# Performance work log

Measured on AMD Instinct MI355X. Metric: run time of the kernel, lower is better.

Reference implementation:

```python
import jax, jax.numpy as jnp
import numpy as np

H = 100      # hidden size
L = 4096     # sequence length


def setup_inputs() -> dict:
    key = jax.random.key(0)
    ks = jax.random.split(key, 11)
    s = 1.0 / np.sqrt(H)
    u = lambda k, sh: jax.random.uniform(k, sh, jnp.float32, -s, s)
    return {
        "input_seq": jax.random.normal(ks[0], (L,), jnp.float32),
        "W_ih_l0": u(ks[1], (4 * H, 1)),
        "W_hh_l0": u(ks[2], (4 * H, H)),
        "b_ih_l0": u(ks[3], (4 * H,)),
        "b_hh_l0": u(ks[4], (4 * H,)),
        "W_ih_l1": u(ks[5], (4 * H, H)),
        "W_hh_l1": u(ks[6], (4 * H, H)),
        "b_ih_l1": u(ks[7], (4 * H,)),
        "b_hh_l1": u(ks[8], (4 * H,)),
        "W_lin": u(ks[9], (1, H)),
        "b_lin": u(ks[10], (1,)),
    }


def _lstm_layer(x, Wih, Whh, bih, bhh):
    # x: [L, B, in] -> hs: [L, B, H]. PyTorch gate order: i, f, g, o.
    h_dim = Wih.shape[0] // 4
    b = bih + bhh

    def step(carry, xt):
        h, c = carry
        gates = xt @ Wih.T + h @ Whh.T + b          # [B, 4H]
        i, f, g, o = jnp.split(gates, 4, axis=-1)
        c = jax.nn.sigmoid(f) * c + jax.nn.sigmoid(i) * jnp.tanh(g)
        h = jax.nn.sigmoid(o) * jnp.tanh(c)
        return (h, c), h

    B = x.shape[1]
    h0 = jnp.zeros((B, h_dim), x.dtype)
    c0 = jnp.zeros((B, h_dim), x.dtype)
    _, hs = jax.lax.scan(step, (h0, c0), x)
    return hs


def reference(input_seq, W_ih_l0, W_hh_l0, b_ih_l0, b_hh_l0,
              W_ih_l1, W_hh_l1, b_ih_l1, b_hh_l1, W_lin, b_lin):
    x = input_seq.reshape(-1, 1, 1)                 # [L, B=1, 1]
    h1 = _lstm_layer(x, W_ih_l0, W_hh_l0, b_ih_l0, b_hh_l0)   # [L,1,H]
    h2 = _lstm_layer(h1, W_ih_l1, W_hh_l1, b_ih_l1, b_hh_l1)  # [L,1,H]
    preds = h2.reshape(h2.shape[0], -1) @ W_lin.T + b_lin      # [L,1]
    return preds[-1]                                 # [1]
```

## Files before the change

### kernel.cpp

```cpp
#include <hip/hip_runtime.h>

#define HH 100
#define LL 4096
#define NT 512

#define WS_H1_FLOATS (LL*128)
#define WS_NEEDED ((size_t)WS_H1_FLOATS*4 + (size_t)LL*4)

typedef float v2f __attribute__((ext_vector_type(2)));
__device__ __forceinline__ v2f fma2(v2f a, v2f b, v2f c) { return __builtin_elementwise_fma(a, b, c); }
__device__ __forceinline__ v2f v2c(float2 f) { v2f r; r.x = f.x; r.y = f.y; return r; }

__device__ __forceinline__ float sigmoidf_(float x) { return 1.0f / (1.0f + __expf(-x)); }
__device__ __forceinline__ float tanhf_(float x)    { return 1.0f - 2.0f / (__expf(2.0f * x) + 1.0f); }

#define DECLROW(n) v2f n##_0,n##_1,n##_2,n##_3,n##_4,n##_5,n##_6,n##_7,n##_8,n##_9,n##_10,n##_11, \
                       n##_12,n##_13,n##_14,n##_15,n##_16,n##_17,n##_18,n##_19,n##_20,n##_21,n##_22,n##_23,n##_24;
#define LOADROW(n, P) { const float2* q2_ = reinterpret_cast<const float2*>(P); \
  n##_0=v2c(q2_[0]);   n##_1=v2c(q2_[1]);   n##_2=v2c(q2_[2]);   n##_3=v2c(q2_[3]);   n##_4=v2c(q2_[4]); \
  n##_5=v2c(q2_[5]);   n##_6=v2c(q2_[6]);   n##_7=v2c(q2_[7]);   n##_8=v2c(q2_[8]);   n##_9=v2c(q2_[9]); \
  n##_10=v2c(q2_[10]); n##_11=v2c(q2_[11]); n##_12=v2c(q2_[12]); n##_13=v2c(q2_[13]); n##_14=v2c(q2_[14]); \
  n##_15=v2c(q2_[15]); n##_16=v2c(q2_[16]); n##_17=v2c(q2_[17]); n##_18=v2c(q2_[18]); n##_19=v2c(q2_[19]); \
  n##_20=v2c(q2_[20]); n##_21=v2c(q2_[21]); n##_22=v2c(q2_[22]); n##_23=v2c(q2_[23]); n##_24=v2c(q2_[24]); }

#define STEP2(j,p,q) { float4 hv = hb4[j]; v2f hl, hh; hl.x=hv.x; hl.y=hv.y; hh.x=hv.z; hh.y=hv.w; \
  a0=fma2(wa_##p,hl,a0); a0=fma2(wa_##q,hh,a0); \
  a1=fma2(wb_##p,hl,a1); a1=fma2(wb_##q,hh,a1); }

#define STEP4(j,p,q) { float4 hv = hb4[j]; v2f hl, hh; hl.x=hv.x; hl.y=hv.y; hh.x=hv.z; hh.y=hv.w; \
  a0=fma2(wa_##p,hl,a0); a0=fma2(wa_##q,hh,a0); \
  a1=fma2(wb_##p,hl,a1); a1=fma2(wb_##q,hh,a1); \
  a2=fma2(wc_##p,hl,a2); a2=fma2(wc_##q,hh,a2); \
  a3=fma2(wd_##p,hl,a3); a3=fma2(wd_##q,hh,a3); }

#define P_LDS_FLOATS 5120

__global__ __attribute__((amdgpu_flat_work_group_size(NT, NT)))
           __attribute__((amdgpu_waves_per_eu(2, 2)))
void lstm_pipe2(const float* __restrict__ x_seq,  const float* __restrict__ Wih0,
                const float* __restrict__ Whh0,   const float* __restrict__ bih0,
                const float* __restrict__ bhh0,   const float* __restrict__ Wih1,
                const float* __restrict__ Whh1,   const float* __restrict__ bih1,
                const float* __restrict__ bhh1,   const float* __restrict__ Wlin,
                const float* __restrict__ blin,   float* __restrict__ ws_h1,
                int* __restrict__ ws_flag,        float* __restrict__ out)
{
    extern __shared__ float lds[];
    const int tid = threadIdx.x;

    if (blockIdx.x == 0) {
        float* x_s   = lds;
        float* h1_s  = lds + 4096;
        float* part0 = lds + 4200;

        const int half = tid & 1;
        const int q    = tid >> 1;
        const bool act = (q < 200);
        const int r0   = act ? 2*q : 0;

        {   const float4* src = reinterpret_cast<const float4*>(x_seq);
            float4* dst = reinterpret_cast<float4*>(x_s);
            for (int i = tid; i < LL/4; i += NT) dst[i] = src[i]; }
        if (tid < 104) h1_s[tid] = 0.0f;

        DECLROW(wa) DECLROW(wb)
        LOADROW(wa, Whh0 + (r0+0)*HH + half*50)
        LOADROW(wb, Whh0 + (r0+1)*HH + half*50)
        float bw0 = 0.f, bw1 = 0.f;
        if (act) {
            if (half == 0) { bw0 = bih0[r0] + bhh0[r0]; bw1 = bih0[r0+1] + bhh0[r0+1]; }
            else           { bw0 = Wih0[r0];            bw1 = Wih0[r0+1]; }
        }
        const float4* hb4 = reinterpret_cast<const float4*>(h1_s + half*52);
        float c0 = 0.0f;
        __syncthreads();

        for (int t = 0; t < LL; ++t) {
            const float xt  = x_s[t];
            const float xvs = half ? xt : 1.0f;
            if (act) {
                v2f a0 = {0.f,0.f}, a1 = {0.f,0.f};
                STEP2(0,0,1)   STEP2(1,2,3)   STEP2(2,4,5)   STEP2(3,6,7)
                STEP2(4,8,9)   STEP2(5,10,11) STEP2(6,12,13) STEP2(7,14,15)
                STEP2(8,16,17) STEP2(9,18,19) STEP2(10,20,21) STEP2(11,22,23)
                { float4 hv = hb4[12]; v2f hl; hl.x = hv.x; hl.y = hv.y;
                  a0 = fma2(wa_24, hl, a0); a1 = fma2(wb_24, hl, a1); }
                float* pw = part0 + half*400 + r0;
                pw[0] = fmaf(bw0, xvs, a0.x + a0.y);
                pw[1] = fmaf(bw1, xvs, a1.x + a1.y);
            }
            __syncthreads();
            if (tid < 100) {
                const int j = tid;
                float G0 = part0[j]       + part0[400 + j];
                float G1 = part0[j + 100] + part0[500 + j];
                float G2 = part0[j + 200] + part0[600 + j];
                float G3 = part0[j + 300] + part0[700 + j];
                c0 = sigmoidf_(G1)*c0 + sigmoidf_(G0)*tanhf_(G2);
                float h = sigmoidf_(G3)*tanhf_(c0);
                h1_s[j + 2*(j >= 50)] = h;
                __hip_atomic_store(&ws_h1[t*128 + j], h, __ATOMIC_RELAXED, __HIP_MEMORY_SCOPE_AGENT);
            }
            __syncthreads();
            if (tid == 0)
                __hip_atomic_store(&ws_flag[t], 1, __ATOMIC_RELEASE, __HIP_MEMORY_SCOPE_AGENT);
        }
    } else {
        float* h1c   = lds;
        float* h2_s  = lds + 104;
        float* part1 = lds + 208;
        float* red   = lds + 1808;

        const bool dotter = (tid < 400);
        const int  c    = dotter ? (tid / 200) : 0;
        const int  rem  = dotter ? (tid % 200) : 0;
        const int  half = rem / 100;
        const int  b    = rem % 100;
        const int  rb   = 4*b;
        const float* mat = c ? Whh1 : Wih1;

        DECLROW(wa) DECLROW(wb) DECLROW(wc) DECLROW(wd)
        LOADROW(wa, mat + (rb+0)*HH + half*50)
        LOADROW(wb, mat + (rb+1)*HH + half*50)
        LOADROW(wc, mat + (rb+2)*HH + half*50)
        LOADROW(wd, mat + (rb+3)*HH + half*50)
        float bw0=0.f, bw1=0.f, bw2=0.f, bw3=0.f;
        if (dotter && c == 0 && half == 0) {
            bw0 = bih1[rb]   + bhh1[rb];
            bw1 = bih1[rb+1] + bhh1[rb+1];
            bw2 = bih1[rb+2] + bhh1[rb+2];
            bw3 = bih1[rb+3] + bhh1[rb+3];
        }
        const float4* hb4 = reinterpret_cast<const float4*>((c ? h2_s : h1c) + half*52);
        const int pbase = half*800 + c*400 + rb;

        const bool gl = (tid >= 400) && (tid < 500);
        const int  j  = tid - 400;
        const float wl = gl ? Wlin[j] : 0.0f;
        float c1 = 0.0f;

        if (tid < 104) { h1c[tid] = 0.0f; h2_s[tid] = 0.0f; }
        __syncthreads();
        if (gl) {
            while (__hip_atomic_load(&ws_flag[0], __ATOMIC_ACQUIRE, __HIP_MEMORY_SCOPE_AGENT) == 0) {}
            float h0 = __hip_atomic_load(&ws_h1[j], __ATOMIC_RELAXED, __HIP_MEMORY_SCOPE_AGENT);
            h1c[j + 2*(j >= 50)] = h0;
            while (__hip_atomic_load(&ws_flag[1], __ATOMIC_ACQUIRE, __HIP_MEMORY_SCOPE_AGENT) == 0) {}
        }
        __syncthreads();

        for (int t = 0; t < LL; ++t) {
            float hnf = 0.0f; int f2v = 1;
            if (gl) {
                const int tp1 = (t+1 < LL) ? t+1 : LL-1;
                const int tp2 = (t+2 < LL) ? t+2 : LL-1;
                hnf = __hip_atomic_load(&ws_h1[tp1*128 + j], __ATOMIC_RELAXED, __HIP_MEMORY_SCOPE_AGENT);
                f2v = __hip_atomic_load(&ws_flag[tp2], __ATOMIC_ACQUIRE, __HIP_MEMORY_SCOPE_AGENT);
            }
            if (dotter) {
                v2f a0 = {0.f,0.f}, a1 = {0.f,0.f}, a2 = {0.f,0.f}, a3 = {0.f,0.f};
                STEP4(0,0,1)   STEP4(1,2,3)   STEP4(2,4,5)   STEP4(3,6,7)
                STEP4(4,8,9)   STEP4(5,10,11) STEP4(6,12,13) STEP4(7,14,15)
                STEP4(8,16,17) STEP4(9,18,19) STEP4(10,20,21) STEP4(11,22,23)
                { float4 hv = hb4[12]; v2f hl; hl.x = hv.x; hl.y = hv.y;
                  a0 = fma2(wa_24, hl, a0); a1 = fma2(wb_24, hl, a1);
                  a2 = fma2(wc_24, hl, a2); a3 = fma2(wd_24, hl, a3); }
                reinterpret_cast<float4*>(part1 + pbase)[0] =
                    make_float4(a0.x + a0.y + bw0, a1.x + a1.y + bw1,
                                a2.x + a2.y + bw2, a3.x + a3.y + bw3);
            }
            __syncthreads();
            if (gl) {
                float G0 = (part1[j]       + part1[800+j])       + (part1[400+j]       + part1[1200+j]);
                float G1 = (part1[j+100]   + part1[900+j])       + (part1[500+j]       + part1[1300+j]);
                float G2 = (part1[j+200]   + part1[1000+j])      + (part1[600+j]       + part1[1400+j]);
                float G3 = (part1[j+300]   + part1[1100+j])      + (part1[700+j]       + part1[1500+j]);
                c1 = sigmoidf_(G1)*c1 + sigmoidf_(G0)*tanhf_(G2);
                h2_s[j + 2*(j >= 50)] = sigmoidf_(G3)*tanhf_(c1);
                h1c[j + 2*(j >= 50)] = hnf;
                while (f2v == 0) {
                    const int tp2 = (t+2 < LL) ? t+2 : LL-1;
                    f2v = __hip_atomic_load(&ws_flag[tp2], __ATOMIC_ACQUIRE, __HIP_MEMORY_SCOPE_AGENT);
                }
            }
            __syncthreads();
        }
        if (gl) red[j] = wl * h2_s[j + 2*(j >= 50)];
        __syncthreads();
        if (tid == 0) {
            float s = blin[0];
            for (int k = 0; k < HH; ++k) s += red[k];
            out[0] = s;
        }
    }
}

#define NLDSROW 176
#define RB0  176
#define WQ_OFF   4096
#define H1_OFF   (WQ_OFF + 2*NLDSROW*52)
#define H2_OFF   (H1_OFF + 104)
#define PART_OFF (H2_OFF + 104)
#define Q_OFF    (PART_OFF + 2048)
#define LDS_FLOATS (Q_OFF + 352)

#define TSK(j) { float4 wv = tp4[j]; float4 hv = hb4t[j]; v2f wl_,wh_,hl_,hh_; \
  wl_.x=wv.x; wl_.y=wv.y; wh_.x=wv.z; wh_.y=wv.w; hl_.x=hv.x; hl_.y=hv.y; hh_.x=hv.z; hh_.y=hv.w; \
  tq=fma2(wl_,hl_,tq); tq=fma2(wh_,hh_,tq); }

__global__ __attribute__((amdgpu_flat_work_group_size(NT, NT)))
           __attribute__((amdgpu_waves_per_eu(2, 2)))
void lstm_v256_kernel(const float* __restrict__ x_seq, const float* __restrict__ Wih0,
                      const float* __restrict__ Whh0,  const float* __restrict__ bih0,
                      const float* __restrict__ bhh0,  const float* __restrict__ Wih1,
                      const float* __restrict__ Whh1,  const float* __restrict__ bih1,
                      const float* __restrict__ bhh1,  const float* __restrict__ Wlin,
                      const float* __restrict__ blin,  float* __restrict__ out)
{
    extern __shared__ float lds[];
    float* x_s    = lds;
    float* wq     = lds + WQ_OFF;
    float* h1_s   = lds + H1_OFF;
    float* h2_s   = lds + H2_OFF;
    float* part_s = lds + PART_OFF;
    float* q_s    = lds + Q_OFF;

    const int tid  = threadIdx.x;
    const int half = tid & 1;
    const int qid  = tid >> 1;
    const int rowbase = RB0 + 4*qid;

    {   const float4* src = reinterpret_cast<const float4*>(x_seq);
        float4* dst = reinterpret_cast<float4*>(x_s);
        for (int i = tid; i < LL/4; i += NT) dst[i] = src[i]; }
    for (int idx = tid; idx < 2*NLDSROW*50; idx += NT) {
        int hf  = idx / (NLDSROW*50);
        int rem = idx - hf*(NLDSROW*50);
        int row = rem / 50;
        int cc  = rem - row*50;
        wq[(hf*NLDSROW + row)*52 + cc] = Whh0[row*HH + hf*50 + cc];
    }
    if (tid < 104) { h1_s[tid] = 0.0f; h2_s[tid] = 0.0f; }

    const float* M; int r0;
    if (rowbase < 400)      { M = Whh0; r0 = rowbase; }
    else if (rowbase < 800) { M = Wih1; r0 = rowbase - 400; }
    else                    { M = Whh1; r0 = rowbase - 800; }

    DECLROW(wa) DECLROW(wb) DECLROW(wc) DECLROW(wd)
    LOADROW(wa, M + (r0+0)*HH + half*50)
    LOADROW(wb, M + (r0+1)*HH + half*50)
    LOADROW(wc, M + (r0+2)*HH + half*50)
    LOADROW(wd, M + (r0+3)*HH + half*50)

    float bw0, bw1, bw2, bw3;
    {
        const int ra = rowbase, rb = rowbase+1, rc = rowbase+2, rd = rowbase+3;
        if (half == 0) {
            bw0 = (ra < 400) ? (bih0[ra] + bhh0[ra]) : (ra < 800) ? (bih1[ra-400] + bhh1[ra-400]) : 0.0f;
            bw1 = (rb < 400) ? (bih0[rb] + bhh0[rb]) : (rb < 800) ? (bih1[rb-400] + bhh1[rb-400]) : 0.0f;
            bw2 = (rc < 400) ? (bih0[rc] + bhh0[rc]) : (rc < 800) ? (bih1[rc-400] + bhh1[rc-400]) : 0.0f;
            bw3 = (rd < 400) ? (bih0[rd] + bhh0[rd]) : (rd < 800) ? (bih1[rd-400] + bhh1[rd-400]) : 0.0f;
        } else {
            bw0 = (ra < 400) ? Wih0[ra] : 0.0f;
            bw1 = (rb < 400) ? Wih0[rb] : 0.0f;
            bw2 = (rc < 400) ? Wih0[rc] : 0.0f;
            bw3 = (rd < 400) ? Wih0[rd] : 0.0f;
        }
    }

    float lb = 0.0f;
    if (tid < 2*NLDSROW) lb = half ? Wih0[qid] : (bih0[qid] + bhh0[qid]);
    const float4* tp4  = reinterpret_cast<const float4*>(wq + (half*NLDSROW + qid)*52);
    const float4* hb4t = reinterpret_cast<const float4*>(h1_s + half*52);
    const float4* hb4  = reinterpret_cast<const float4*>(((rowbase < 800) ? h1_s : h2_s) + half*52);

    const float wl = (tid < HH) ? Wlin[tid] : 0.0f;
    const int slotbase = qid + half*1024;
    float c0 = 0.0f, c1 = 0.0f;
    __syncthreads();

    for (int t = 0; t <= LL; ++t) {
        const float xt  = x_s[(t < LL) ? t : (LL-1)];
        const float xvs = half ? xt : 1.0f;
        {
            v2f a0 = {0.f,0.f}, a1 = {0.f,0.f}, a2 = {0.f,0.f}, a3 = {0.f,0.f};
            STEP4(0,0,1)   STEP4(1,2,3)   STEP4(2,4,5)   STEP4(3,6,7)
            STEP4(4,8,9)   STEP4(5,10,11) STEP4(6,12,13) STEP4(7,14,15)
            STEP4(8,16,17) STEP4(9,18,19) STEP4(10,20,21) STEP4(11,22,23)
            { float4 hv = hb4[12]; v2f hl; hl.x = hv.x; hl.y = hv.y;
              a0 = fma2(wa_24, hl, a0); a1 = fma2(wb_24, hl, a1);
              a2 = fma2(wc_24, hl, a2); a3 = fma2(wd_24, hl, a3); }
            part_s[slotbase + 0*256] = fmaf(bw0, xvs, a0.x + a0.y);
            part_s[slotbase + 1*256] = fmaf(bw1, xvs, a1.x + a1.y);
            part_s[slotbase + 2*256] = fmaf(bw2, xvs, a2.x + a2.y);
            part_s[slotbase + 3*256] = fmaf(bw3, xvs, a3.x + a3.y);
        }
        if (tid < 2*NLDSROW) {
            v2f tq = {0.f,0.f};
            TSK(0) TSK(1) TSK(2) TSK(3) TSK(4) TSK(5)
            TSK(6) TSK(7) TSK(8) TSK(9) TSK(10) TSK(11)
            { float4 wv = tp4[12]; float4 hv = hb4t[12];
              v2f wl_, hl_; wl_.x = wv.x; wl_.y = wv.y; hl_.x = hv.x; hl_.y = hv.y;
              tq = fma2(wl_, hl_, tq); }
            q_s[qid + half*NLDSROW] = fmaf(lb, xvs, tq.x + tq.y);
        }
        __syncthreads();
        if (tid < HH) {
            const int jj = tid;
            float g[4];
            #pragma unroll
            for (int k = 0; k < 4; ++k) {
                int r = jj + k*100;
                if (r < NLDSROW) g[k] = q_s[r] + q_s[r + NLDSROW];
                else { int rr = r - RB0; int bb = (rr >> 2) + ((rr & 3) << 8);
                       g[k] = part_s[bb] + part_s[bb + 1024]; }
            }
            if (t < LL) {
                c0 = sigmoidf_(g[1])*c0 + sigmoidf_(g[0])*tanhf_(g[2]);
                h1_s[jj + 2*(jj >= 50)] = sigmoidf_(g[3])*tanhf_(c0);
            }
        } else if (tid >= 128 && tid < 128 + HH) {
            if (t >= 1) {
                const int jj = tid - 128;
                float v[4];
                #pragma unroll
                for (int k = 0; k < 4; ++k) {
                    int g1i = jj + k*100;
                    int rr1 = (400 + g1i) - RB0; int b1i = (rr1 >> 2) + ((rr1 & 3) << 8);
                    int rr2 = (800 + g1i) - RB0; int b2i = (rr2 >> 2) + ((rr2 & 3) << 8);
                    v[k] = (part_s[b1i] + part_s[b1i + 1024]) + (part_s[b2i] + part_s[b2i + 1024]);
                }
                c1 = sigmoidf_(v[1])*c1 + sigmoidf_(v[0])*tanhf_(v[2]);
                h2_s[jj + 2*(jj >= 50)] = sigmoidf_(v[3])*tanhf_(c1);
            }
        }
        __syncthreads();
    }
    if (tid < HH) part_s[tid] = wl * h2_s[tid + 2*(tid >= 50)];
    __syncthreads();
    if (tid == 0) {
        float s = 0.0f;
        for (int k = 0; k < HH; ++k) s += part_s[k];
        out[0] = s + blin[0];
    }
}

extern "C" void kernel_launch(void* const* d_in, const int* in_sizes, int n_in,
                              void* d_out, int out_size, void* d_ws, size_t ws_size,
                              hipStream_t stream) {
    (void)in_sizes; (void)n_in; (void)out_size;

    const float* x_seq = (const float*)d_in[0];
    const float* Wih0  = (const float*)d_in[1];
    const float* Whh0  = (const float*)d_in[2];
    const float* bih0  = (const float*)d_in[3];
    const float* bhh0  = (const float*)d_in[4];
    const float* Wih1  = (const float*)d_in[5];
    const float* Whh1  = (const float*)d_in[6];
    const float* bih1  = (const float*)d_in[7];
    const float* bhh1  = (const float*)d_in[8];
    const float* Wlin  = (const float*)d_in[9];
    const float* blin  = (const float*)d_in[10];
    float* out = (float*)d_out;

    if (d_ws != nullptr && ws_size >= WS_NEEDED) {
        float* ws_h1  = (float*)d_ws;
        int*   ws_flg = (int*)((char*)d_ws + (size_t)WS_H1_FLOATS*4);
        hipMemsetAsync(ws_flg, 0, LL*sizeof(int), stream);
        hipLaunchKernelGGL(lstm_pipe2, dim3(2), dim3(NT),
                           P_LDS_FLOATS*sizeof(float), stream,
                           x_seq, Wih0, Whh0, bih0, bhh0,
                           Wih1, Whh1, bih1, bhh1, Wlin, blin,
                           ws_h1, ws_flg, out);
    } else {
        static bool attr_set = false;
        if (!attr_set) {
            hipFuncSetAttribute((const void*)lstm_v256_kernel,
                                hipFuncAttributeMaxDynamicSharedMemorySize,
                                LDS_FLOATS * (int)sizeof(float));
            attr_set = true;
        }
        hipLaunchKernelGGL(lstm_v256_kernel, dim3(1), dim3(NT),
                           LDS_FLOATS * sizeof(float), stream,
                           x_seq, Wih0, Whh0, bih0, bhh0,
                           Wih1, Whh1, bih1, bhh1, Wlin, blin, out);
    }
}
```

Before: 4.281 ms.

## Split layer-1 LSTM into separate input-projection and recurrent blocks in a 3-stage pipeline

Moves from a two-block pipeline to three blocks. Block 0 runs the layer-0 recurrence. Block 1 computes the layer-1 input projection (Wih1·h1) and streams the pre-activations through a ring buffer in global memory. Block 2 runs only the layer-1 recurrent matvec (Whh1·h2) plus the gate math. The goal is to halve the per-step work on the layer-1 critical path, which previously did both matvecs with four rows per thread. In exchange it adds a second inter-block handoff with acquire/release flags, ring-buffer backpressure counters, and extra global traffic of 800 floats per step. The fallback single-block kernel is also removed.

```diff
diff --git a/kernel.cpp b/kernel.cpp
--- a/kernel.cpp
+++ b/kernel.cpp
@@ -3,9 +3,8 @@
 #define HH 100
 #define LL 4096
 #define NT 512
-
-#define WS_H1_FLOATS (LL*128)
-#define WS_NEEDED ((size_t)WS_H1_FLOATS*4 + (size_t)LL*4)
+#define RH 512
+#define BPLAG 504
 
 typedef float v2f __attribute__((ext_vector_type(2)));
 __device__ __forceinline__ v2f fma2(v2f a, v2f b, v2f c) { return __builtin_elementwise_fma(a, b, c); }
@@ -26,14 +25,229 @@
 #define STEP2(j,p,q) { float4 hv = hb4[j]; v2f hl, hh; hl.x=hv.x; hl.y=hv.y; hh.x=hv.z; hh.y=hv.w; \
   a0=fma2(wa_##p,hl,a0); a0=fma2(wa_##q,hh,a0); \
   a1=fma2(wb_##p,hl,a1); a1=fma2(wb_##q,hh,a1); }
+#define DOT2TAIL { float4 hv = hb4[12]; v2f hl; hl.x = hv.x; hl.y = hv.y; \
+  a0 = fma2(wa_24, hl, a0); a1 = fma2(wb_24, hl, a1); }
+#define DOT2ALL  STEP2(0,0,1) STEP2(1,2,3) STEP2(2,4,5) STEP2(3,6,7) STEP2(4,8,9) STEP2(5,10,11) \
+                 STEP2(6,12,13) STEP2(7,14,15) STEP2(8,16,17) STEP2(9,18,19) STEP2(10,20,21) STEP2(11,22,23) DOT2TAIL
+
+#define AST(p,v) __hip_atomic_store((p), (v), __ATOMIC_RELAXED, __HIP_MEMORY_SCOPE_AGENT)
+#define ALD(p)   __hip_atomic_load((p), __ATOMIC_RELAXED, __HIP_MEMORY_SCOPE_AGENT)
+#define AFLAGST(p) __hip_atomic_store((p), 1, __ATOMIC_RELEASE, __HIP_MEMORY_SCOPE_AGENT)
+#define AFLAGLD(p) __hip_atomic_load((p), __ATOMIC_ACQUIRE, __HIP_MEMORY_SCOPE_AGENT)
+
+#define P3_LDS_FLOATS 5120
+
+__global__ __attribute__((amdgpu_flat_work_group_size(NT, NT)))
+           __attribute__((amdgpu_waves_per_eu(2, 2)))
+void lstm_pipe3(const float* __restrict__ x_seq,  const float* __restrict__ Wih0,
+                const float* __restrict__ Whh0,   const float* __restrict__ bih0,
+                const float* __restrict__ bhh0,   const float* __restrict__ Wih1,
+                const float* __restrict__ Whh1,   const float* __restrict__ bih1,
+                const float* __restrict__ bhh1,   const float* __restrict__ Wlin,
+                const float* __restrict__ blin,
+                float* __restrict__ ws_h1,  float* __restrict__ ws_p01,
+                int* __restrict__ flag0,    int* __restrict__ flag1,
+                int* __restrict__ cons1,    int* __restrict__ cons2,
+                float* __restrict__ out)
+{
+    extern __shared__ float lds[];
+    const int tid  = threadIdx.x;
+    const int half = tid & 1;
+    const int q    = tid >> 1;
+    const bool act = (q < 200);
+    const int r0   = act ? 2*q : 0;
+
+    if (blockIdx.x == 0) {
+        float* x_s   = lds;
+        float* h1_s  = lds + 4096;
+        float* part0 = lds + 4200;
+
+        {   const float4* src = reinterpret_cast<const float4*>(x_seq);
+            float4* dst = reinterpret_cast<float4*>(x_s);
+            for (int i = tid; i < LL/4; i += NT) dst[i] = src[i]; }
+        if (tid < 104) h1_s[tid] = 0.0f;
+
+        DECLROW(wa) DECLROW(wb)
+        LOADROW(wa, Whh0 + (r0+0)*HH + half*50)
+        LOADROW(wb, Whh0 + (r0+1)*HH + half*50)
+        float bw0 = 0.f, bw1 = 0.f;
+        if (act) {
+            if (half == 0) { bw0 = bih0[r0] + bhh0[r0]; bw1 = bih0[r0+1] + bhh0[r0+1]; }
+            else           { bw0 = Wih0[r0];            bw1 = Wih0[r0+1]; }
+        }
+        const float4* hb4 = reinterpret_cast<const float4*>(h1_s + half*52);
+        float c0 = 0.0f;
+        __syncthreads();
+
+        for (int t = 0; t < LL; ++t) {
+            const float xt  = x_s[t];
+            const float xvs = half ? xt : 1.0f;
+            if (act) {
+                v2f a0 = {0.f,0.f}, a1 = {0.f,0.f};
+                DOT2ALL
+                float* pw = part0 + half*400 + r0;
+                pw[0] = fmaf(bw0, xvs, a0.x + a0.y);
+                pw[1] = fmaf(bw1, xvs, a1.x + a1.y);
+            }
+            __syncthreads();
+            if (tid < 100) {
+                const int j = tid;
+                float G0 = part0[j]       + part0[400 + j];
+                float G1 = part0[j + 100] + part0[500 + j];
+                float G2 = part0[j + 200] + part0[600 + j];
+                float G3 = part0[j + 300] + part0[700 + j];
+                c0 = sigmoidf_(G1)*c0 + sigmoidf_(G0)*tanhf_(G2);
+                float h = sigmoidf_(G3)*tanhf_(c0);
+                h1_s[j + 2*(j >= 50)] = h;
+                AST(&ws_h1[(t & (RH-1))*128 + j], h);
+            }
+            __syncthreads();
+            if (tid == 0) {
+                AFLAGST(&flag0[t]);
+                if (t >= BPLAG + 1) {
+                    while (ALD(cons1) < t - BPLAG) {}
+                }
+            }
+        }
+    } else if (blockIdx.x == 1) {
+        float* h1c = lds;
+
+        DECLROW(wa) DECLROW(wb)
+        LOADROW(wa, Wih1 + (r0+0)*HH + half*50)
+        LOADROW(wb, Wih1 + (r0+1)*HH + half*50)
+        float bw0 = 0.f, bw1 = 0.f;
+        if (act && half == 0) { bw0 = bih1[r0] + bhh1[r0]; bw1 = bih1[r0+1] + bhh1[r0+1]; }
+
+        const bool gl = (tid >= 400) && (tid < 500);
+        const int  j  = tid - 400;
+        if (tid < 104) h1c[tid] = 0.0f;
+        __syncthreads();
+
+        if (gl) {
+            while (AFLAGLD(&flag0[0]) == 0) {}
+            h1c[j + 2*(j >= 50)] = ALD(&ws_h1[j]);
+            while (AFLAGLD(&flag0[1]) == 0) {}
+        }
+        __syncthreads();
+        const float4* hb4 = reinterpret_cast<const float4*>(h1c + half*52);
+
+        for (int t = 0; t < LL; ++t) {
+            float hnf = 0.0f; int f2v = 1;
+            if (gl) {
+                const int tp1 = (t+1 < LL) ? t+1 : LL-1;
+                const int tp2 = (t+2 < LL) ? t+2 : LL-1;
+                hnf = ALD(&ws_h1[(tp1 & (RH-1))*128 + j]);
+                f2v = AFLAGLD(&flag0[tp2]);
+            }
+            if (act) {
+                v2f a0 = {0.f,0.f}, a1 = {0.f,0.f};
+                DOT2ALL
+                const int base = (t & (RH-1))*800 + half*400 + r0;
+                AST(&ws_p01[base],     a0.x + a0.y + bw0);
+                AST(&ws_p01[base + 1], a1.x + a1.y + bw1);
+            }
+            __syncthreads();
+            if (gl) {
+                h1c[j + 2*(j >= 50)] = hnf;
+                while (f2v == 0) {
+                    const int tp2 = (t+2 < LL) ? t+2 : LL-1;
+                    f2v = AFLAGLD(&flag0[tp2]);
+                }
+            }
+            if (tid == 0) {
+                AFLAGST(&flag1[t]);
+                AST(cons1, t);
+                if (t >= BPLAG + 1) {
+                    while (ALD(cons2) < t - BPLAG) {}
+                }
+            }
+            __syncthreads();
+        }
+    } else {
+        float* h2_s  = lds;
+        float* part2 = lds + 104;
+        float* red   = lds + 904;
+
+        DECLROW(wa) DECLROW(wb)
+        LOADROW(wa, Whh1 + (r0+0)*HH + half*50)
+        LOADROW(wb, Whh1 + (r0+1)*HH + half*50)
+
+        const bool gl = (tid >= 400) && (tid < 500);
+        const int  j  = tid - 400;
+        const float wl = gl ? Wlin[j] : 0.0f;
+        float c1 = 0.0f;
+        float pc0=0.f,pc1=0.f,pc2=0.f,pc3=0.f,pc4=0.f,pc5=0.f,pc6=0.f,pc7=0.f;
+
+        if (tid < 104) h2_s[tid] = 0.0f;
+        __syncthreads();
+
+        if (gl) {
+            while (AFLAGLD(&flag1[0]) == 0) {}
+            pc0 = ALD(&ws_p01[j]);        pc1 = ALD(&ws_p01[100 + j]);
+            pc2 = ALD(&ws_p01[200 + j]);  pc3 = ALD(&ws_p01[300 + j]);
+            pc4 = ALD(&ws_p01[400 + j]);  pc5 = ALD(&ws_p01[500 + j]);
+            pc6 = ALD(&ws_p01[600 + j]);  pc7 = ALD(&ws_p01[700 + j]);
+            while (AFLAGLD(&flag1[1]) == 0) {}
+        }
+        __syncthreads();
+        const float4* hb4 = reinterpret_cast<const float4*>(h2_s + half*52);
+
+        for (int t = 0; t < LL; ++t) {
+            float pn0=0.f,pn1=0.f,pn2=0.f,pn3=0.f,pn4=0.f,pn5=0.f,pn6=0.f,pn7=0.f;
+            int f2v = 1;
+            if (gl) {
+                const int tp1 = (t+1 < LL) ? t+1 : LL-1;
+                const int tp2 = (t+2 < LL) ? t+2 : LL-1;
+                const int b = (tp1 & (RH-1))*800;
+                pn0 = ALD(&ws_p01[b + j]);        pn1 = ALD(&ws_p01[b + 100 + j]);
+                pn2 = ALD(&ws_p01[b + 200 + j]);  pn3 = ALD(&ws_p01[b + 300 + j]);
+                pn4 = ALD(&ws_p01[b + 400 + j]);  pn5 = ALD(&ws_p01[b + 500 + j]);
+                pn6 = ALD(&ws_p01[b + 600 + j]);  pn7 = ALD(&ws_p01[b + 700 + j]);
+                f2v = AFLAGLD(&flag1[tp2]);
+            }
+            if (act) {
+                v2f a0 = {0.f,0.f}, a1 = {0.f,0.f};
+                DOT2ALL
+                float* pw = part2 + half*400 + r0;
+                pw[0] = a0.x + a0.y;
+                pw[1] = a1.x + a1.y;
+            }
+            __syncthreads();
+            if (gl) {
+                float G0 = (part2[j]       + part2[400 + j]) + (pc0 + pc4);
+                float G1 = (part2[100 + j] + part2[500 + j]) + (pc1 + pc5);
+                float G2 = (part2[200 + j] + part2[600 + j]) + (pc2 + pc6);
+                float G3 = (part2[300 + j] + part2[700 + j]) + (pc3 + pc7);
+                c1 = sigmoidf_(G1)*c1 + sigmoidf_(G0)*tanhf_(G2);
+                h2_s[j + 2*(j >= 50)] = sigmoidf_(G3)*tanhf_(c1);
+                pc0=pn0; pc1=pn1; pc2=pn2; pc3=pn3; pc4=pn4; pc5=pn5; pc6=pn6; pc7=pn7;
+                while (f2v == 0) {
+                    const int tp2 = (t+2 < LL) ? t+2 : LL-1;
+                    f2v = AFLAGLD(&flag1[tp2]);
+                }
+            }
+            if (tid == 0) AST(cons2, t);
+            __syncthreads();
+        }
+        if (gl) red[j] = wl * h2_s[j + 2*(j >= 50)];
+        __syncthreads();
+        if (tid == 0) {
+            float s = blin[0];
+            for (int k = 0; k < HH; ++k) s += red[k];
+            out[0] = s;
+        }
+    }
+}
+
+#define WS_H1_FLOATS (LL*128)
+#define WS2_NEEDED ((size_t)WS_H1_FLOATS*4 + (size_t)LL*4)
+#define P_LDS_FLOATS 5120
 
 #define STEP4(j,p,q) { float4 hv = hb4[j]; v2f hl, hh; hl.x=hv.x; hl.y=hv.y; hh.x=hv.z; hh.y=hv.w; \
   a0=fma2(wa_##p,hl,a0); a0=fma2(wa_##q,hh,a0); \
   a1=fma2(wb_##p,hl,a1); a1=fma2(wb_##q,hh,a1); \
   a2=fma2(wc_##p,hl,a2); a2=fma2(wc_##q,hh,a2); \
   a3=fma2(wd_##p,hl,a3); a3=fma2(wd_##q,hh,a3); }
-
-#define P_LDS_FLOATS 5120
 
 __global__ __attribute__((amdgpu_flat_work_group_size(NT, NT)))
            __attribute__((amdgpu_waves_per_eu(2, 2)))
@@ -80,11 +294,7 @@
             const float xvs = half ? xt : 1.0f;
             if (act) {
                 v2f a0 = {0.f,0.f}, a1 = {0.f,0.f};
-                STEP2(0,0,1)   STEP2(1,2,3)   STEP2(2,4,5)   STEP2(3,6,7)
-                STEP2(4,8,9)   STEP2(5,10,11) STEP2(6,12,13) STEP2(7,14,15)
-                STEP2(8,16,17) STEP2(9,18,19) STEP2(10,20,21) STEP2(11,22,23)
-                { float4 hv = hb4[12]; v2f hl; hl.x = hv.x; hl.y = hv.y;
-                  a0 = fma2(wa_24, hl, a0); a1 = fma2(wb_24, hl, a1); }
+                DOT2ALL
                 float* pw = part0 + half*400 + r0;
                 pw[0] = fmaf(bw0, xvs, a0.x + a0.y);
                 pw[1] = fmaf(bw1, xvs, a1.x + a1.y);
@@ -99,11 +309,10 @@
                 c0 = sigmoidf_(G1)*c0 + sigmoidf_(G0)*tanhf_(G2);
                 float h = sigmoidf_(G3)*tanhf_(c0);
                 h1_s[j + 2*(j >= 50)] = h;
-                __hip_atomic_store(&ws_h1[t*128 + j], h, __ATOMIC_RELAXED, __HIP_MEMORY_SCOPE_AGENT);
-            }
-            __syncthreads();
-            if (tid == 0)
-                __hip_atomic_store(&ws_flag[t], 1, __ATOMIC_RELEASE, __HIP_MEMORY_SCOPE_AGENT);
+                AST(&ws_h1[t*128 + j], h);
+            }
+            __syncthreads();
+            if (tid == 0) AFLAGST(&ws_flag[t]);
         }
     } else {
         float* h1c   = lds;
@@ -142,10 +351,9 @@
         if (tid < 104) { h1c[tid] = 0.0f; h2_s[tid] = 0.0f; }
         __syncthreads();
         if (gl) {
-            while (__hip_atomic_load(&ws_flag[0], __ATOMIC_ACQUIRE, __HIP_MEMORY_SCOPE_AGENT) == 0) {}
-            float h0 = __hip_atomic_load(&ws_h1[j], __ATOMIC_RELAXED, __HIP_MEMORY_SCOPE_AGENT);
-            h1c[j + 2*(j >= 50)] = h0;
-            while (__hip_atomic_load(&ws_flag[1], __ATOMIC_ACQUIRE, __HIP_MEMORY_SCOPE_AGENT) == 0) {}
+            while (AFLAGLD(&ws_flag[0]) == 0) {}
+            h1c[j + 2*(j >= 50)] = ALD(&ws_h1[j]);
+            while (AFLAGLD(&ws_flag[1]) == 0) {}
         }
         __syncthreads();
 
@@ -154,8 +362,8 @@
             if (gl) {
                 const int tp1 = (t+1 < LL) ? t+1 : LL-1;
                 const int tp2 = (t+2 < LL) ? t+2 : LL-1;
-                hnf = __hip_atomic_load(&ws_h1[tp1*128 + j], __ATOMIC_RELAXED, __HIP_MEMORY_SCOPE_AGENT);
-                f2v = __hip_atomic_load(&ws_flag[tp2], __ATOMIC_ACQUIRE, __HIP_MEMORY_SCOPE_AGENT);
+                hnf = ALD(&ws_h1[tp1*128 + j]);
+                f2v = AFLAGLD(&ws_flag[tp2]);
             }
             if (dotter) {
                 v2f a0 = {0.f,0.f}, a1 = {0.f,0.f}, a2 = {0.f,0.f}, a3 = {0.f,0.f};
@@ -171,16 +379,16 @@
             }
             __syncthreads();
             if (gl) {
-                float G0 = (part1[j]       + part1[800+j])       + (part1[400+j]       + part1[1200+j]);
-                float G1 = (part1[j+100]   + part1[900+j])       + (part1[500+j]       + part1[1300+j]);
-                float G2 = (part1[j+200]   + part1[1000+j])      + (part1[600+j]       + part1[1400+j]);
-                float G3 = (part1[j+300]   + part1[1100+j])      + (part1[700+j]       + part1[1500+j]);
+                float G0 = (part1[j]       + part1[800+j])  + (part1[400+j]  + part1[1200+j]);
+                float G1 = (part1[j+100]   + part1[900+j])  + (part1[500+j]  + part1[1300+j]);
+                float G2 = (part1[j+200]   + part1[1000+j]) + (part1[600+j]  + part1[1400+j]);
+                float G3 = (part1[j+300]   + part1[1100+j]) + (part1[700+j]  + part1[1500+j]);
                 c1 = sigmoidf_(G1)*c1 + sigmoidf_(G0)*tanhf_(G2);
                 h2_s[j + 2*(j >= 50)] = sigmoidf_(G3)*tanhf_(c1);
                 h1c[j + 2*(j >= 50)] = hnf;
                 while (f2v == 0) {
                     const int tp2 = (t+2 < LL) ? t+2 : LL-1;
-                    f2v = __hip_atomic_load(&ws_flag[tp2], __ATOMIC_ACQUIRE, __HIP_MEMORY_SCOPE_AGENT);
+                    f2v = AFLAGLD(&ws_flag[tp2]);
                 }
             }
             __syncthreads();
@@ -192,157 +400,6 @@
             for (int k = 0; k < HH; ++k) s += red[k];
             out[0] = s;
         }
-    }
-}
-
-#define NLDSROW 176
-#define RB0  176
-#define WQ_OFF   4096
-#define H1_OFF   (WQ_OFF + 2*NLDSROW*52)
-#define H2_OFF   (H1_OFF + 104)
-#define PART_OFF (H2_OFF + 104)
-#define Q_OFF    (PART_OFF + 2048)
-#define LDS_FLOATS (Q_OFF + 352)
-
-#define TSK(j) { float4 wv = tp4[j]; float4 hv = hb4t[j]; v2f wl_,wh_,hl_,hh_; \
-  wl_.x=wv.x; wl_.y=wv.y; wh_.x=wv.z; wh_.y=wv.w; hl_.x=hv.x; hl_.y=hv.y; hh_.x=hv.z; hh_.y=hv.w; \
-  tq=fma2(wl_,hl_,tq); tq=fma2(wh_,hh_,tq); }
-
-__global__ __attribute__((amdgpu_flat_work_group_size(NT, NT)))
-           __attribute__((amdgpu_waves_per_eu(2, 2)))
-void lstm_v256_kernel(const float* __restrict__ x_seq, const float* __restrict__ Wih0,
-                      const float* __restrict__ Whh0,  const float* __restrict__ bih0,
-                      const float* __restrict__ bhh0,  const float* __restrict__ Wih1,
-                      const float* __restrict__ Whh1,  const float* __restrict__ bih1,
-                      const float* __restrict__ bhh1,  const float* __restrict__ Wlin,
-                      const float* __restrict__ blin,  float* __restrict__ out)
-{
-    extern __shared__ float lds[];
-    float* x_s    = lds;
-    float* wq     = lds + WQ_OFF;
-    float* h1_s   = lds + H1_OFF;
-    float* h2_s   = lds + H2_OFF;
-    float* part_s = lds + PART_OFF;
-    float* q_s    = lds + Q_OFF;
-
-    const int tid  = threadIdx.x;
-    const int half = tid & 1;
-    const int qid  = tid >> 1;
-    const int rowbase = RB0 + 4*qid;
-
-    {   const float4* src = reinterpret_cast<const float4*>(x_seq);
-        float4* dst = reinterpret_cast<float4*>(x_s);
-        for (int i = tid; i < LL/4; i += NT) dst[i] = src[i]; }
-    for (int idx = tid; idx < 2*NLDSROW*50; idx += NT) {
-        int hf  = idx / (NLDSROW*50);
-        int rem = idx - hf*(NLDSROW*50);
-        int row = rem / 50;
-        int cc  = rem - row*50;
-        wq[(hf*NLDSROW + row)*52 + cc] = Whh0[row*HH + hf*50 + cc];
-    }
-    if (tid < 104) { h1_s[tid] = 0.0f; h2_s[tid] = 0.0f; }
-
-    const float* M; int r0;
-    if (rowbase < 400)      { M = Whh0; r0 = rowbase; }
-    else if (rowbase < 800) { M = Wih1; r0 = rowbase - 400; }
-    else                    { M = Whh1; r0 = rowbase - 800; }
-
-    DECLROW(wa) DECLROW(wb) DECLROW(wc) DECLROW(wd)
-    LOADROW(wa, M + (r0+0)*HH + half*50)
-    LOADROW(wb, M + (r0+1)*HH + half*50)
-    LOADROW(wc, M + (r0+2)*HH + half*50)
-    LOADROW(wd, M + (r0+3)*HH + half*50)
-
-    float bw0, bw1, bw2, bw3;
-    {
-        const int ra = rowbase, rb = rowbase+1, rc = rowbase+2, rd = rowbase+3;
-        if (half == 0) {
-            bw0 = (ra < 400) ? (bih0[ra] + bhh0[ra]) : (ra < 800) ? (bih1[ra-400] + bhh1[ra-400]) : 0.0f;
-            bw1 = (rb < 400) ? (bih0[rb] + bhh0[rb]) : (rb < 800) ? (bih1[rb-400] + bhh1[rb-400]) : 0.0f;
-            bw2 = (rc < 400) ? (bih0[rc] + bhh0[rc]) : (rc < 800) ? (bih1[rc-400] + bhh1[rc-400]) : 0.0f;
-            bw3 = (rd < 400) ? (bih0[rd] + bhh0[rd]) : (rd < 800) ? (bih1[rd-400] + bhh1[rd-400]) : 0.0f;
-        } else {
-            bw0 = (ra < 400) ? Wih0[ra] : 0.0f;
-            bw1 = (rb < 400) ? Wih0[rb] : 0.0f;
-            bw2 = (rc < 400) ? Wih0[rc] : 0.0f;
-            bw3 = (rd < 400) ? Wih0[rd] : 0.0f;
-        }
-    }
-
-    float lb = 0.0f;
-    if (tid < 2*NLDSROW) lb = half ? Wih0[qid] : (bih0[qid] + bhh0[qid]);
-    const float4* tp4  = reinterpret_cast<const float4*>(wq + (half*NLDSROW + qid)*52);
-    const float4* hb4t = reinterpret_cast<const float4*>(h1_s + half*52);
-    const float4* hb4  = reinterpret_cast<const float4*>(((rowbase < 800) ? h1_s : h2_s) + half*52);
-
-    const float wl = (tid < HH) ? Wlin[tid] : 0.0f;
-    const int slotbase = qid + half*1024;
-    float c0 = 0.0f, c1 = 0.0f;
-    __syncthreads();
-
-    for (int t = 0; t <= LL; ++t) {
-        const float xt  = x_s[(t < LL) ? t : (LL-1)];
-        const float xvs = half ? xt : 1.0f;
-        {
-            v2f a0 = {0.f,0.f}, a1 = {0.f,0.f}, a2 = {0.f,0.f}, a3 = {0.f,0.f};
-            STEP4(0,0,1)   STEP4(1,2,3)   STEP4(2,4,5)   STEP4(3,6,7)
-            STEP4(4,8,9)   STEP4(5,10,11) STEP4(6,12,13) STEP4(7,14,15)
-            STEP4(8,16,17) STEP4(9,18,19) STEP4(10,20,21) STEP4(11,22,23)
-            { float4 hv = hb4[12]; v2f hl; hl.x = hv.x; hl.y = hv.y;
-              a0 = fma2(wa_24, hl, a0); a1 = fma2(wb_24, hl, a1);
-              a2 = fma2(wc_24, hl, a2); a3 = fma2(wd_24, hl, a3); }
-            part_s[slotbase + 0*256] = fmaf(bw0, xvs, a0.x + a0.y);
-            part_s[slotbase + 1*256] = fmaf(bw1, xvs, a1.x + a1.y);
-            part_s[slotbase + 2*256] = fmaf(bw2, xvs, a2.x + a2.y);
-            part_s[slotbase + 3*256] = fmaf(bw3, xvs, a3.x + a3.y);
-        }
-        if (tid < 2*NLDSROW) {
-            v2f tq = {0.f,0.f};
-            TSK(0) TSK(1) TSK(2) TSK(3) TSK(4) TSK(5)
-            TSK(6) TSK(7) TSK(8) TSK(9) TSK(10) TSK(11)
-            { float4 wv = tp4[12]; float4 hv = hb4t[12];
-              v2f wl_, hl_; wl_.x = wv.x; wl_.y = wv.y; hl_.x = hv.x; hl_.y = hv.y;
-              tq = fma2(wl_, hl_, tq); }
-            q_s[qid + half*NLDSROW] = fmaf(lb, xvs, tq.x + tq.y);
-        }
-        __syncthreads();
-        if (tid < HH) {
-            const int jj = tid;
-            float g[4];
-            #pragma unroll
-            for (int k = 0; k < 4; ++k) {
-                int r = jj + k*100;
-                if (r < NLDSROW) g[k] = q_s[r] + q_s[r + NLDSROW];
-                else { int rr = r - RB0; int bb = (rr >> 2) + ((rr & 3) << 8);
-                       g[k] = part_s[bb] + part_s[bb + 1024]; }
-            }
-            if (t < LL) {
-                c0 = sigmoidf_(g[1])*c0 + sigmoidf_(g[0])*tanhf_(g[2]);
-                h1_s[jj + 2*(jj >= 50)] = sigmoidf_(g[3])*tanhf_(c0);
-            }
-        } else if (tid >= 128 && tid < 128 + HH) {
-            if (t >= 1) {
-                const int jj = tid - 128;
-                float v[4];
-                #pragma unroll
-                for (int k = 0; k < 4; ++k) {
-                    int g1i = jj + k*100;
-                    int rr1 = (400 + g1i) - RB0; int b1i = (rr1 >> 2) + ((rr1 & 3) << 8);
-                    int rr2 = (800 + g1i) - RB0; int b2i = (rr2 >> 2) + ((rr2 & 3) << 8);
-                    v[k] = (part_s[b1i] + part_s[b1i + 1024]) + (part_s[b2i] + part_s[b2i + 1024]);
-                }
-                c1 = sigmoidf_(v[1])*c1 + sigmoidf_(v[0])*tanhf_(v[2]);
-                h2_s[jj + 2*(jj >= 50)] = sigmoidf_(v[3])*tanhf_(c1);
-            }
-        }
-        __syncthreads();
-    }
-    if (tid < HH) part_s[tid] = wl * h2_s[tid + 2*(tid >= 50)];
-    __syncthreads();
-    if (tid == 0) {
-        float s = 0.0f;
-        for (int k = 0; k < HH; ++k) s += part_s[k];
-        out[0] = s + blin[0];
     }
 }
 
@@ -364,7 +421,28 @@
     const float* blin  = (const float*)d_in[10];
     float* out = (float*)d_out;
 
-    if (d_ws != nullptr && ws_size >= WS_NEEDED) {
+    const size_t o_h1  = 0;
+    const size_t o_p01 = (size_t)RH*128*4;
+    const size_t o_f0  = o_p01 + (size_t)RH*800*4;
+    const size_t o_f1  = o_f0 + (size_t)LL*4;
+    const size_t o_c1  = o_f1 + (size_t)LL*4;
+    const size_t o_c2  = o_c1 + 64;
+    const size_t ws3_needed = o_c2 + 64;
+
+    if (d_ws != nullptr && ws_size >= ws3_needed) {
+        float* ws_h1  = (float*)((char*)d_ws + o_h1);
+        float* ws_p01 = (float*)((char*)d_ws + o_p01);
+        int*   flag0  = (int*)((char*)d_ws + o_f0);
+        int*   flag1  = (int*)((char*)d_ws + o_f1);
+        int*   cons1  = (int*)((char*)d_ws + o_c1);
+        int*   cons2  = (int*)((char*)d_ws + o_c2);
+        hipMemsetAsync(flag0, 0, (size_t)LL*8 + 128, stream);
+        hipLaunchKernelGGL(lstm_pipe3, dim3(3), dim3(NT),
+                           P3_LDS_FLOATS*sizeof(float), stream,
+                           x_seq, Wih0, Whh0, bih0, bhh0,
+                           Wih1, Whh1, bih1, bhh1, Wlin, blin,
+                           ws_h1, ws_p01, flag0, flag1, cons1, cons2, out);
+    } else {
         float* ws_h1  = (float*)d_ws;
         int*   ws_flg = (int*)((char*)d_ws + (size_t)WS_H1_FLOATS*4);
         hipMemsetAsync(ws_flg, 0, LL*sizeof(int), stream);
@@ -373,17 +451,5 @@
                            x_seq, Wih0, Whh0, bih0, bhh0,
                            Wih1, Whh1, bih1, bhh1, Wlin, blin,
                            ws_h1, ws_flg, out);
-    } else {
-        static bool attr_set = false;
-        if (!attr_set) {
-            hipFuncSetAttribute((const void*)lstm_v256_kernel,
-                                hipFuncAttributeMaxDynamicSharedMemorySize,
-                                LDS_FLOATS * (int)sizeof(float));
-            attr_set = true;
-        }
-        hipLaunchKernelGGL(lstm_v256_kernel, dim3(1), dim3(NT),
-                           LDS_FLOATS * sizeof(float), stream,
-                           x_seq, Wih0, Whh0, bih0, bhh0,
-                           Wih1, Whh1, bih1, bhh1, Wlin, blin, out);
     }
 }
```

New measurement: 6.459 ms. +50.9%, slower.

## Split layer-1 dot products: recurrent part first, input projection off critical path

Applied to the files above, without the earlier changes.

In the layer-1 block, each thread pair now owns two gate rows of both Whh1 and Wih1. The recurrent Whh1·h2 dot runs before the barrier. The Wih1·h1 projection for the next step is computed after the barrier, into a double-buffered slot, while the gate threads finish the current step. The h1 prefetch now waits on the t+2 flag and keeps two buffered h1 vectors, which removes the spin loop after the gate update. This shortens the serial dependency per timestep, at the cost of more LDS buffers and a different work split.

```diff
diff --git a/kernel.cpp b/kernel.cpp
--- a/kernel.cpp
+++ b/kernel.cpp
@@ -26,12 +26,23 @@
 #define STEP2(j,p,q) { float4 hv = hb4[j]; v2f hl, hh; hl.x=hv.x; hl.y=hv.y; hh.x=hv.z; hh.y=hv.w; \
   a0=fma2(wa_##p,hl,a0); a0=fma2(wa_##q,hh,a0); \
   a1=fma2(wb_##p,hl,a1); a1=fma2(wb_##q,hh,a1); }
-
-#define STEP4(j,p,q) { float4 hv = hb4[j]; v2f hl, hh; hl.x=hv.x; hl.y=hv.y; hh.x=hv.z; hh.y=hv.w; \
-  a0=fma2(wa_##p,hl,a0); a0=fma2(wa_##q,hh,a0); \
-  a1=fma2(wb_##p,hl,a1); a1=fma2(wb_##q,hh,a1); \
-  a2=fma2(wc_##p,hl,a2); a2=fma2(wc_##q,hh,a2); \
-  a3=fma2(wd_##p,hl,a3); a3=fma2(wd_##q,hh,a3); }
+#define DOT2TAIL { float4 hv = hb4[12]; v2f hl; hl.x = hv.x; hl.y = hv.y; \
+  a0 = fma2(wa_24, hl, a0); a1 = fma2(wb_24, hl, a1); }
+#define DOT2ALL  STEP2(0,0,1) STEP2(1,2,3) STEP2(2,4,5) STEP2(3,6,7) STEP2(4,8,9) STEP2(5,10,11) \
+                 STEP2(6,12,13) STEP2(7,14,15) STEP2(8,16,17) STEP2(9,18,19) STEP2(10,20,21) STEP2(11,22,23) DOT2TAIL
+
+#define WSTEP2(j,p,q) { float4 hv = hb4[j]; v2f hl, hh; hl.x=hv.x; hl.y=hv.y; hh.x=hv.z; hh.y=hv.w; \
+  a0=fma2(wc_##p,hl,a0); a0=fma2(wc_##q,hh,a0); \
+  a1=fma2(wd_##p,hl,a1); a1=fma2(wd_##q,hh,a1); }
+#define WDOT2TAIL { float4 hv = hb4[12]; v2f hl; hl.x = hv.x; hl.y = hv.y; \
+  a0 = fma2(wc_24, hl, a0); a1 = fma2(wd_24, hl, a1); }
+#define WDOT2ALL WSTEP2(0,0,1) WSTEP2(1,2,3) WSTEP2(2,4,5) WSTEP2(3,6,7) WSTEP2(4,8,9) WSTEP2(5,10,11) \
+                 WSTEP2(6,12,13) WSTEP2(7,14,15) WSTEP2(8,16,17) WSTEP2(9,18,19) WSTEP2(10,20,21) WSTEP2(11,22,23) WDOT2TAIL
+
+#define AST(p,v) __hip_atomic_store((p), (v), __ATOMIC_RELAXED, __HIP_MEMORY_SCOPE_AGENT)
+#define ALD(p)   __hip_atomic_load((p), __ATOMIC_RELAXED, __HIP_MEMORY_SCOPE_AGENT)
+#define AFLAGST(p) __hip_atomic_store((p), 1, __ATOMIC_RELEASE, __HIP_MEMORY_SCOPE_AGENT)
+#define AFLAGLD(p) __hip_atomic_load((p), __ATOMIC_ACQUIRE, __HIP_MEMORY_SCOPE_AGENT)
 
 #define P_LDS_FLOATS 5120
 
@@ -80,11 +91,7 @@
             const float xvs = half ? xt : 1.0f;
             if (act) {
                 v2f a0 = {0.f,0.f}, a1 = {0.f,0.f};
-                STEP2(0,0,1)   STEP2(1,2,3)   STEP2(2,4,5)   STEP2(3,6,7)
-                STEP2(4,8,9)   STEP2(5,10,11) STEP2(6,12,13) STEP2(7,14,15)
-                STEP2(8,16,17) STEP2(9,18,19) STEP2(10,20,21) STEP2(11,22,23)
-                { float4 hv = hb4[12]; v2f hl; hl.x = hv.x; hl.y = hv.y;
-                  a0 = fma2(wa_24, hl, a0); a1 = fma2(wb_24, hl, a1); }
+                DOT2ALL
                 float* pw = part0 + half*400 + r0;
                 pw[0] = fmaf(bw0, xvs, a0.x + a0.y);
                 pw[1] = fmaf(bw1, xvs, a1.x + a1.y);
@@ -99,92 +106,98 @@
                 c0 = sigmoidf_(G1)*c0 + sigmoidf_(G0)*tanhf_(G2);
                 float h = sigmoidf_(G3)*tanhf_(c0);
                 h1_s[j + 2*(j >= 50)] = h;
-                __hip_atomic_store(&ws_h1[t*128 + j], h, __ATOMIC_RELAXED, __HIP_MEMORY_SCOPE_AGENT);
+                AST(&ws_h1[t*128 + j], h);
             }
             __syncthreads();
-            if (tid == 0)
-                __hip_atomic_store(&ws_flag[t], 1, __ATOMIC_RELEASE, __HIP_MEMORY_SCOPE_AGENT);
+            if (tid == 0) AFLAGST(&ws_flag[t]);
         }
     } else {
-        float* h1c   = lds;
-        float* h2_s  = lds + 104;
-        float* part1 = lds + 208;
-        float* red   = lds + 1808;
-
-        const bool dotter = (tid < 400);
-        const int  c    = dotter ? (tid / 200) : 0;
-        const int  rem  = dotter ? (tid % 200) : 0;
-        const int  half = rem / 100;
-        const int  b    = rem % 100;
-        const int  rb   = 4*b;
-        const float* mat = c ? Whh1 : Wih1;
-
-        DECLROW(wa) DECLROW(wb) DECLROW(wc) DECLROW(wd)
-        LOADROW(wa, mat + (rb+0)*HH + half*50)
-        LOADROW(wb, mat + (rb+1)*HH + half*50)
-        LOADROW(wc, mat + (rb+2)*HH + half*50)
-        LOADROW(wd, mat + (rb+3)*HH + half*50)
-        float bw0=0.f, bw1=0.f, bw2=0.f, bw3=0.f;
-        if (dotter && c == 0 && half == 0) {
-            bw0 = bih1[rb]   + bhh1[rb];
-            bw1 = bih1[rb+1] + bhh1[rb+1];
-            bw2 = bih1[rb+2] + bhh1[rb+2];
-            bw3 = bih1[rb+3] + bhh1[rb+3];
-        }
-        const float4* hb4 = reinterpret_cast<const float4*>((c ? h2_s : h1c) + half*52);
-        const int pbase = half*800 + c*400 + rb;
+        float* h1c  = lds;
+        float* h2_s = lds + 208;
+        float* pwhh = lds + 312;
+        float* pwih = lds + 1112;
+        float* red  = lds + 2712;
+
+        const int half = tid & 1;
+        const int q    = tid >> 1;
+        const bool act = (q < 200);
+        const int r0   = act ? 2*q : 0;
+
+        DECLROW(wa) DECLROW(wb)
+        DECLROW(wc) DECLROW(wd)
+        LOADROW(wa, Whh1 + (r0+0)*HH + half*50)
+        LOADROW(wb, Whh1 + (r0+1)*HH + half*50)
+        LOADROW(wc, Wih1 + (r0+0)*HH + half*50)
+        LOADROW(wd, Wih1 + (r0+1)*HH + half*50)
+        float bw0 = 0.f, bw1 = 0.f;
+        if (act && half == 0) { bw0 = bih1[r0] + bhh1[r0]; bw1 = bih1[r0+1] + bhh1[r0+1]; }
 
         const bool gl = (tid >= 400) && (tid < 500);
         const int  j  = tid - 400;
         const float wl = gl ? Wlin[j] : 0.0f;
         float c1 = 0.0f;
 
-        if (tid < 104) { h1c[tid] = 0.0f; h2_s[tid] = 0.0f; }
-        __syncthreads();
+        if (tid < 208) h1c[tid] = 0.0f;
+        if (tid < 104) h2_s[tid] = 0.0f;
+        __syncthreads();
+
         if (gl) {
-            while (__hip_atomic_load(&ws_flag[0], __ATOMIC_ACQUIRE, __HIP_MEMORY_SCOPE_AGENT) == 0) {}
-            float h0 = __hip_atomic_load(&ws_h1[j], __ATOMIC_RELAXED, __HIP_MEMORY_SCOPE_AGENT);
-            h1c[j + 2*(j >= 50)] = h0;
-            while (__hip_atomic_load(&ws_flag[1], __ATOMIC_ACQUIRE, __HIP_MEMORY_SCOPE_AGENT) == 0) {}
+            while (AFLAGLD(&ws_flag[0]) == 0) {}
+            h1c[j + 2*(j >= 50)] = ALD(&ws_h1[j]);
+            while (AFLAGLD(&ws_flag[1]) == 0) {}
+            h1c[104 + j + 2*(j >= 50)] = ALD(&ws_h1[128 + j]);
+        }
+        __syncthreads();
+        if (act) {
+            const float4* hb4 = reinterpret_cast<const float4*>(h1c + half*52);
+            v2f a0 = {0.f,0.f}, a1 = {0.f,0.f};
+            WDOT2ALL
+            float* pw = pwih + half*400 + r0;
+            pw[0] = a0.x + a0.y + bw0;
+            pw[1] = a1.x + a1.y + bw1;
         }
         __syncthreads();
 
         for (int t = 0; t < LL; ++t) {
-            float hnf = 0.0f; int f2v = 1;
+            const int cur = t & 1, nxt = cur ^ 1;
+            float hnf = 0.0f;
+
+            if (act) {
+                const float4* hb4 = reinterpret_cast<const float4*>(h2_s + half*52);
+                v2f a0 = {0.f,0.f}, a1 = {0.f,0.f};
+                DOT2ALL
+                float* pw = pwhh + half*400 + r0;
+                pw[0] = a0.x + a0.y;
+                pw[1] = a1.x + a1.y;
+            }
             if (gl) {
-                const int tp1 = (t+1 < LL) ? t+1 : LL-1;
                 const int tp2 = (t+2 < LL) ? t+2 : LL-1;
-                hnf = __hip_atomic_load(&ws_h1[tp1*128 + j], __ATOMIC_RELAXED, __HIP_MEMORY_SCOPE_AGENT);
-                f2v = __hip_atomic_load(&ws_flag[tp2], __ATOMIC_ACQUIRE, __HIP_MEMORY_SCOPE_AGENT);
-            }
-            if (dotter) {
-                v2f a0 = {0.f,0.f}, a1 = {0.f,0.f}, a2 = {0.f,0.f}, a3 = {0.f,0.f};
-                STEP4(0,0,1)   STEP4(1,2,3)   STEP4(2,4,5)   STEP4(3,6,7)
-                STEP4(4,8,9)   STEP4(5,10,11) STEP4(6,12,13) STEP4(7,14,15)
-                STEP4(8,16,17) STEP4(9,18,19) STEP4(10,20,21) STEP4(11,22,23)
-                { float4 hv = hb4[12]; v2f hl; hl.x = hv.x; hl.y = hv.y;
-                  a0 = fma2(wa_24, hl, a0); a1 = fma2(wb_24, hl, a1);
-                  a2 = fma2(wc_24, hl, a2); a3 = fma2(wd_24, hl, a3); }
-                reinterpret_cast<float4*>(part1 + pbase)[0] =
-                    make_float4(a0.x + a0.y + bw0, a1.x + a1.y + bw1,
-                                a2.x + a2.y + bw2, a3.x + a3.y + bw3);
+                while (AFLAGLD(&ws_flag[tp2]) == 0) {}
+                hnf = ALD(&ws_h1[tp2*128 + j]);
             }
             __syncthreads();
+
+            if (act) {
+                const float4* hb4 = reinterpret_cast<const float4*>(h1c + nxt*104 + half*52);
+                v2f a0 = {0.f,0.f}, a1 = {0.f,0.f};
+                WDOT2ALL
+                float* pw = pwih + nxt*800 + half*400 + r0;
+                pw[0] = a0.x + a0.y + bw0;
+                pw[1] = a1.x + a1.y + bw1;
+            }
             if (gl) {
-                float G0 = (part1[j]       + part1[800+j])       + (part1[400+j]       + part1[1200+j]);
-                float G1 = (part1[j+100]   + part1[900+j])       + (part1[500+j]       + part1[1300+j]);
-                float G2 = (part1[j+200]   + part1[1000+j])      + (part1[600+j]       + part1[1400+j]);
-                float G3 = (part1[j+300]   + part1[1100+j])      + (part1[700+j]       + part1[1500+j]);
+                const float* pc = pwih + cur*800;
+                float G0 = (pwhh[j]       + pwhh[400 + j]) + (pc[j]       + pc[400 + j]);
+                float G1 = (pwhh[100 + j] + pwhh[500 + j]) + (pc[100 + j] + pc[500 + j]);
+                float G2 = (pwhh[200 + j] + pwhh[600 + j]) + (pc[200 + j] + pc[600 + j]);
+                float G3 = (pwhh[300 + j] + pwhh[700 + j]) + (pc[300 + j] + pc[700 + j]);
                 c1 = sigmoidf_(G1)*c1 + sigmoidf_(G0)*tanhf_(G2);
                 h2_s[j + 2*(j >= 50)] = sigmoidf_(G3)*tanhf_(c1);
-                h1c[j + 2*(j >= 50)] = hnf;
-                while (f2v == 0) {
-                    const int tp2 = (t+2 < LL) ? t+2 : LL-1;
-                    f2v = __hip_atomic_load(&ws_flag[tp2], __ATOMIC_ACQUIRE, __HIP_MEMORY_SCOPE_AGENT);
-                }
+                h1c[cur*104 + j + 2*(j >= 50)] = hnf;
             }
             __syncthreads();
         }
+
         if (gl) red[j] = wl * h2_s[j + 2*(j >= 50)];
         __syncthreads();
         if (tid == 0) {
@@ -204,6 +217,11 @@
 #define Q_OFF    (PART_OFF + 2048)
 #define LDS_FLOATS (Q_OFF + 352)
 
+#define STEP4(j,p,q) { float4 hv = hb4[j]; v2f hl, hh; hl.x=hv.x; hl.y=hv.y; hh.x=hv.z; hh.y=hv.w; \
+  a0=fma2(wa_##p,hl,a0); a0=fma2(wa_##q,hh,a0); \
+  a1=fma2(wb_##p,hl,a1); a1=fma2(wb_##q,hh,a1); \
+  a2=fma2(wc_##p,hl,a2); a2=fma2(wc_##q,hh,a2); \
+  a3=fma2(wd_##p,hl,a3); a3=fma2(wd_##q,hh,a3); }
 #define TSK(j) { float4 wv = tp4[j]; float4 hv = hb4t[j]; v2f wl_,wh_,hl_,hh_; \
   wl_.x=wv.x; wl_.y=wv.y; wh_.x=wv.z; wh_.y=wv.w; hl_.x=hv.x; hl_.y=hv.y; hh_.x=hv.z; hh_.y=hv.w; \
   tq=fma2(wl_,hl_,tq); tq=fma2(wh_,hh_,tq); }
```

Measured after the change: 4.575 ms. 1.07x slower.
